# Kernel tuning notes

Measured on AMD Instinct MI355X. Metric: run time of the kernel, lower is better.

Reference implementation:

```python
import jax, jax.numpy as jnp
import numpy as np

PS = 32
D = 256


def setup_inputs() -> dict:
    key = jax.random.key(0)
    ks = jax.random.split(key, 9)
    B, L = 32, 32768
    s_in = 1.0 / np.sqrt(PS)
    s_d = 1.0 / np.sqrt(D)
    return {
        "x": jax.random.normal(ks[0], (B, L), dtype=jnp.float32),
        "W_proj": jax.random.normal(ks[1], (PS, D), dtype=jnp.float32) * s_in,
        "b_proj": jnp.zeros((D,), jnp.float32),
        "W_qkv": jax.random.normal(ks[2], (D, 3 * D), dtype=jnp.float32) * s_d,
        "b_qkv": jnp.zeros((3 * D,), jnp.float32),
        "W_out": jax.random.normal(ks[3], (D, D), dtype=jnp.float32) * s_d,
        "b_out": jnp.zeros((D,), jnp.float32),
        "W_head": jax.random.normal(ks[4], (D, PS), dtype=jnp.float32) * s_d,
        "b_head": jnp.zeros((PS,), jnp.float32),
    }


def reference(x, W_proj, b_proj, W_qkv, b_qkv, W_out, b_out, W_head, b_head):
    B, L = x.shape
    T = L // PS
    # InstanceNorm over full series (torch .std is unbiased -> ddof=1)
    mean = jnp.mean(x, axis=-1, keepdims=True)
    std = jnp.std(x, axis=-1, keepdims=True, ddof=1) + 1e-5
    x_norm = (x - mean) / std
    patches = x_norm.reshape(B, T, PS)
    # Patch embedding
    h = patches @ W_proj + b_proj  # [B, T, D]
    # Single-head causal self-attention (explicit scores, as in source)
    qkv = h @ W_qkv + b_qkv
    q, k, v = jnp.split(qkv, 3, axis=-1)
    scale = 1.0 / jnp.sqrt(jnp.asarray(D, dtype=h.dtype))
    attn = jnp.einsum("btd,bsd->bts", q, k) * scale  # [B, T, T]
    causal = jnp.tril(jnp.ones((T, T), dtype=bool))
    attn = jnp.where(causal, attn, -jnp.inf)
    attn = jax.nn.softmax(attn, axis=-1)
    out = jnp.einsum("bts,bsd->btd", attn, v)
    out = out @ W_out + b_out
    # Prediction head + next-patch MSE loss
    pred = out @ W_head + b_head  # [B, T, PS]
    loss = jnp.mean((pred[:, :-1] - patches[:, 1:]) ** 2)
    return loss
```

## Files before the change

kernel.cpp:

```cpp
#include <hip/hip_runtime.h>
#include <math.h>

#define B_SZ 32
#define L_SZ 32768
#define T_SZ 1024
#define PS_SZ 32
#define D_SZ 256
#define SM_M 10.0f

typedef float f32x4 __attribute__((ext_vector_type(4)));
typedef short s16x8 __attribute__((ext_vector_type(8)));
typedef unsigned short u16x8 __attribute__((ext_vector_type(8)));

__device__ __forceinline__ unsigned short f2bf(float f) {
  union { float f; unsigned int u; } v; v.f = f;
  unsigned int r = v.u + 0x7FFFu + ((v.u >> 16) & 1u);
  return (unsigned short)(r >> 16);
}

__device__ __forceinline__ void g2l16(const unsigned short* g, unsigned short* l) {
  __builtin_amdgcn_global_load_lds(
      (const __attribute__((address_space(1))) unsigned int*)g,
      (__attribute__((address_space(3))) unsigned int*)l, 16, 0, 0);
}

__global__ __launch_bounds__(256) void prep_kernel(const float* __restrict__ x,
                                                   float* __restrict__ sgpart,
                                                   const float* __restrict__ Wp,
                                                   const float* __restrict__ bp,
                                                   const float* __restrict__ Wq,
                                                   const float* __restrict__ bq,
                                                   const float* __restrict__ Wo,
                                                   const float* __restrict__ bo,
                                                   const float* __restrict__ Wh,
                                                   const float* __restrict__ bh,
                                                   float* __restrict__ Wcb,
                                                   unsigned short* __restrict__ WqT,
                                                   unsigned short* __restrict__ WfT,
                                                   float* __restrict__ bfp,
                                                   unsigned int* __restrict__ total,
                                                   float* __restrict__ lsum) {
  __shared__ float red[8];
  const int g = blockIdx.x, tid = threadIdx.x;
  const int w = tid >> 6, lane = tid & 63;
  if (g < 256) {
    const int b = g >> 3;
    const float* p = x + (size_t)b * L_SZ + (size_t)(g & 7) * 4096;
    float s = 0.f, ss = 0.f;
#pragma unroll
    for (int i = 0; i < 4; ++i) {
      float4 f = ((const float4*)p)[tid + i * 256];
      s += f.x + f.y + f.z + f.w;
      ss += f.x * f.x + f.y * f.y + f.z * f.z + f.w * f.w;
    }
#pragma unroll
    for (int off = 32; off >= 1; off >>= 1) {
      s += __shfl_down(s, off);
      ss += __shfl_down(ss, off);
    }
    if (lane == 0) { red[w] = s; red[4 + w] = ss; }
    __syncthreads();
    if (tid == 0) {
      sgpart[g * 2]     = red[0] + red[1] + red[2] + red[3];
      sgpart[g * 2 + 1] = red[4] + red[5] + red[6] + red[7];
    }
  } else if (g < 388) {
    int idx = (g - 256) * 256 + tid;
    if (idx < 33 * 768) {
      int p = idx / 768, j = idx % 768;
      const float* arow = (p < 32) ? (Wp + p * 256) : bp;
      float acc = (p < 32) ? 0.f : bq[j];
      for (int d = 0; d < 256; ++d) acc += arow[d] * Wq[d * 768 + j];
      if (p < 32) WqT[j * 32 + p] = f2bf(acc);
      else Wcb[j] = acc;
    } else {
      int k = idx - 33 * 768;
      if (k < 8192) {
        int p = k >> 8, d = k & 255;
        float acc = 0.f;
        for (int e = 0; e < 256; ++e) acc += Wo[d * 256 + e] * Wh[e * 32 + p];
        WfT[p * 256 + d] = f2bf(acc);
      } else if (k < 8224) {
        int p = k - 8192;
        float acc = bh[p];
        for (int e = 0; e < 256; ++e) acc += bo[e] * Wh[e * 32 + p];
        bfp[p] = acc;
      }
    }
  } else {
    if (tid == 0) { total[0] = 0u; lsum[0] = 0.f; }
  }
}

__global__ __launch_bounds__(256) void qkv_kernel(const float* __restrict__ x,
                                                  const float* __restrict__ sgpart,
                                                  const unsigned short* __restrict__ WqT,
                                                  const float* __restrict__ Wcb,
                                                  unsigned short* __restrict__ Qb,
                                                  unsigned short* __restrict__ Kb,
                                                  unsigned short* __restrict__ Vtt) {
  __shared__ unsigned short T4[4][8448];
  const int tid = threadIdx.x;
  const int w = tid >> 6, lane = tid & 63;
  const int lo = lane & 15, quad = lane >> 4;
  unsigned short* Tw = T4[w];
  const int mbase = blockIdx.x * 128 + w * 32;
  const int b = mbase >> 10;
  float S = 0.f, SS = 0.f;
#pragma unroll
  for (int i = 0; i < 8; ++i) {
    S += sgpart[(b * 8 + i) * 2];
    SS += sgpart[(b * 8 + i) * 2 + 1];
  }
  const float mean = S * (1.f / (float)L_SZ);
  const float var = (SS - S * mean) * (1.f / (float)(L_SZ - 1));
  const float inv = 1.f / (sqrtf(var) + 1e-5f);
  s16x8 af0, af1;
  {
    float4 a = *(const float4*)&x[(size_t)(mbase + lo) * 32 + quad * 8];
    float4 c = *(const float4*)&x[(size_t)(mbase + lo) * 32 + quad * 8 + 4];
    af0[0] = (short)f2bf((a.x - mean) * inv); af0[1] = (short)f2bf((a.y - mean) * inv);
    af0[2] = (short)f2bf((a.z - mean) * inv); af0[3] = (short)f2bf((a.w - mean) * inv);
    af0[4] = (short)f2bf((c.x - mean) * inv); af0[5] = (short)f2bf((c.y - mean) * inv);
    af0[6] = (short)f2bf((c.z - mean) * inv); af0[7] = (short)f2bf((c.w - mean) * inv);
    float4 d = *(const float4*)&x[(size_t)(mbase + 16 + lo) * 32 + quad * 8];
    float4 e = *(const float4*)&x[(size_t)(mbase + 16 + lo) * 32 + quad * 8 + 4];
    af1[0] = (short)f2bf((d.x - mean) * inv); af1[1] = (short)f2bf((d.y - mean) * inv);
    af1[2] = (short)f2bf((d.z - mean) * inv); af1[3] = (short)f2bf((d.w - mean) * inv);
    af1[4] = (short)f2bf((e.x - mean) * inv); af1[5] = (short)f2bf((e.y - mean) * inv);
    af1[6] = (short)f2bf((e.z - mean) * inv); af1[7] = (short)f2bf((e.w - mean) * inv);
  }
#pragma unroll 4
  for (int nt = 0; nt < 16; ++nt) {
    s16x8 bf = *(const s16x8*)&WqT[(size_t)(nt * 16 + lo) * 32 + quad * 8];
    f32x4 c0 = {0.f, 0.f, 0.f, 0.f}, c1 = {0.f, 0.f, 0.f, 0.f};
    c0 = __builtin_amdgcn_mfma_f32_16x16x32_bf16(af0, bf, c0, 0, 0, 0);
    c1 = __builtin_amdgcn_mfma_f32_16x16x32_bf16(af1, bf, c1, 0, 0, 0);
    const int col = nt * 16 + lo;
    const float bi = Wcb[col];
#pragma unroll
    for (int i = 0; i < 4; ++i) {
      Tw[(quad * 4 + i) * 264 + col]      = f2bf((c0[i] + bi) * 0.0625f);
      Tw[(16 + quad * 4 + i) * 264 + col] = f2bf((c1[i] + bi) * 0.0625f);
    }
  }
#pragma unroll
  for (int it = 0; it < 16; ++it) {
    const int gsub = it * 64 + lane;
    const int row = gsub >> 5, c16 = gsub & 31;
    *(u16x8*)&Qb[(size_t)(mbase + row) * 256 + c16 * 8] =
        *(const u16x8*)&Tw[row * 264 + c16 * 8];
  }
#pragma unroll 4
  for (int nt = 0; nt < 16; ++nt) {
    s16x8 bf = *(const s16x8*)&WqT[(size_t)(256 + nt * 16 + lo) * 32 + quad * 8];
    f32x4 c0 = {0.f, 0.f, 0.f, 0.f}, c1 = {0.f, 0.f, 0.f, 0.f};
    c0 = __builtin_amdgcn_mfma_f32_16x16x32_bf16(af0, bf, c0, 0, 0, 0);
    c1 = __builtin_amdgcn_mfma_f32_16x16x32_bf16(af1, bf, c1, 0, 0, 0);
    const int col = nt * 16 + lo;
    const float bi = Wcb[256 + col];
#pragma unroll
    for (int i = 0; i < 4; ++i) {
      Tw[(quad * 4 + i) * 264 + col]      = f2bf(c0[i] + bi);
      Tw[(16 + quad * 4 + i) * 264 + col] = f2bf(c1[i] + bi);
    }
  }
#pragma unroll
  for (int it = 0; it < 16; ++it) {
    const int gsub = it * 64 + lane;
    const int row = gsub >> 5, c16 = gsub & 31;
    *(u16x8*)&Kb[(size_t)(mbase + row) * 256 + c16 * 8] =
        *(const u16x8*)&Tw[row * 264 + c16 * 8];
  }
#pragma unroll 4
  for (int nt2 = 0; nt2 < 16; ++nt2) {
    s16x8 aw = *(const s16x8*)&WqT[(size_t)(512 + nt2 * 16 + lo) * 32 + quad * 8];
    f32x4 c0 = {0.f, 0.f, 0.f, 0.f}, c1 = {0.f, 0.f, 0.f, 0.f};
    c0 = __builtin_amdgcn_mfma_f32_16x16x32_bf16(aw, af0, c0, 0, 0, 0);
    c1 = __builtin_amdgcn_mfma_f32_16x16x32_bf16(aw, af1, c1, 0, 0, 0);
#pragma unroll
    for (int i = 0; i < 4; ++i) {
      const int d = nt2 * 16 + quad * 4 + i;
      const float bv = Wcb[512 + d];
      Tw[d * 32 + lo]      = f2bf(c0[i] + bv);
      Tw[d * 32 + 16 + lo] = f2bf(c1[i] + bv);
    }
  }
  {
    const int ktq = (mbase >> 5) & 31;
    const size_t vb = ((size_t)b * 32 + ktq) * 8192;
#pragma unroll
    for (int it = 0; it < 16; ++it) {
      const int gsub = it * 64 + lane;
      *(u16x8*)&Vtt[vb + gsub * 8] = *(const u16x8*)&Tw[gsub * 8];
    }
  }
}

__global__ __launch_bounds__(256) void attn_kernel(const unsigned short* __restrict__ Qb,
                                                   const unsigned short* __restrict__ Kb,
                                                   const unsigned short* __restrict__ Vtt,
                                                   const unsigned short* __restrict__ WfT,
                                                   const float* __restrict__ bfp,
                                                   const float* __restrict__ x,
                                                   const float* __restrict__ sgpart,
                                                   float* __restrict__ lsum,
                                                   unsigned int* __restrict__ total,
                                                   float* __restrict__ out) {
  __shared__ unsigned short SMEM[35328];
  const int g = blockIdx.x;
  const int j = g >> 3;
  const int b = (g & 7) * 4 + (j & 3);
  const int qt = 15 - (j >> 2);
  const int tid = threadIdx.x;
  const int w = tid >> 6, lane = tid & 63;
  const int lo = lane & 15, quad = lane >> 4;

  const int qr0 = qt * 64 + w * 16;
  const size_t kbase = (size_t)b << 10;

  s16x8 qf[8];
  const size_t qrow = (kbase + qr0 + lo) * 256;
#pragma unroll
  for (int kc = 0; kc < 8; ++kc) qf[kc] = *(const s16x8*)&Qb[qrow + kc * 32 + quad * 8];

  f32x4 O[16];
#pragma unroll
  for (int nt = 0; nt < 16; ++nt) O[nt] = (f32x4){0.f, 0.f, 0.f, 0.f};
  f32x4 Ol = {0.f, 0.f, 0.f, 0.f};
  s16x8 ones;
#pragma unroll
  for (int jj = 0; jj < 8; ++jj) ones[jj] = (short)0x3F80;

  const int c16p = tid & 31;
  const int keyr = tid >> 5;
  const int c16s = (c16p & 24) | ((c16p & 7) ^ keyr);
  const unsigned short* kgp = Kb + (kbase << 8) + keyr * 256 + c16s * 8;
  const int dql = tid >> 2;
  const int cpq = (tid & 3) ^ ((tid >> 3) & 3);
  const unsigned short* vgp = Vtt + (size_t)b * 262144 + dql * 32 + cpq * 8;
  const int ldst = (w * 64) * 8;

  unsigned short* myp = &SMEM[32768 + w * 640];
  const int lo7 = lo & 7;
  const int nk = 2 * (qt + 1);

#pragma unroll
  for (int it = 0; it < 4; ++it) g2l16(kgp + it * 2048, &SMEM[it * 2048 + ldst]);
#pragma unroll
  for (int it = 0; it < 4; ++it) g2l16(vgp + it * 2048, &SMEM[8192 + it * 2048 + ldst]);
  kgp += 8192; vgp += 8192;

  for (int kt = 0; kt < nk; ++kt) {
    const int k0 = kt * 32;
    __syncthreads();
    const int cur = (kt & 1) << 14;
    if (kt + 1 < nk) {
      const int nxt = ((kt + 1) & 1) << 14;
#pragma unroll
      for (int it = 0; it < 4; ++it) g2l16(kgp + it * 2048, &SMEM[nxt + it * 2048 + ldst]);
#pragma unroll
      for (int it = 0; it < 4; ++it)
        g2l16(vgp + it * 2048, &SMEM[nxt + 8192 + it * 2048 + ldst]);
      kgp += 8192; vgp += 8192;
    }

    if (k0 <= qr0 + 15) {
      f32x4 s0 = {0.f, 0.f, 0.f, 0.f}, s1 = {0.f, 0.f, 0.f, 0.f};
#pragma unroll
      for (int kc = 0; kc < 8; ++kc) {
        const int c16 = kc * 4 + quad;
        const int cs = (c16 & 24) | ((c16 & 7) ^ lo7);
        s16x8 kf0 = *(const s16x8*)&SMEM[cur + (lo * 32 + cs) * 8];
        s16x8 kf1 = *(const s16x8*)&SMEM[cur + ((16 + lo) * 32 + cs) * 8];
        s0 = __builtin_amdgcn_mfma_f32_16x16x32_bf16(qf[kc], kf0, s0, 0, 0, 0);
        s1 = __builtin_amdgcn_mfma_f32_16x16x32_bf16(qf[kc], kf1, s1, 0, 0, 0);
      }
      if (k0 + 31 > qr0) {
#pragma unroll
        for (int ii = 0; ii < 4; ++ii) {
          const int row = qr0 + quad * 4 + ii;
          if (k0 + lo > row) s0[ii] = -1e30f;
          if (k0 + 16 + lo > row) s1[ii] = -1e30f;
        }
      }
#pragma unroll
      for (int ii = 0; ii < 4; ++ii) {
        myp[(quad * 4 + ii) * 40 + lo]      = f2bf(__expf(s0[ii] - SM_M));
        myp[(quad * 4 + ii) * 40 + 16 + lo] = f2bf(__expf(s1[ii] - SM_M));
      }
      s16x8 pf = *(const s16x8*)&myp[lo * 40 + quad * 8];
      Ol = __builtin_amdgcn_mfma_f32_16x16x32_bf16(pf, ones, Ol, 0, 0, 0);
#pragma unroll
      for (int nt = 0; nt < 16; ++nt) {
        const int d = nt * 16 + lo;
        const int cp = quad ^ ((d >> 1) & 3);
        s16x8 vf = *(const s16x8*)&SMEM[cur + 8192 + ((d << 2) + cp) * 8];
        O[nt] = __builtin_amdgcn_mfma_f32_16x16x32_bf16(pf, vf, O[nt], 0, 0, 0);
      }
    }
  }
  __syncthreads();

  float inv4[4];
#pragma unroll
  for (int ii = 0; ii < 4; ++ii) inv4[ii] = 1.f / Ol[ii];
  unsigned short* OLw = &SMEM[w * 4224];
#pragma unroll
  for (int nt = 0; nt < 16; ++nt)
#pragma unroll
    for (int ii = 0; ii < 4; ++ii)
      OLw[(quad * 4 + ii) * 264 + nt * 16 + lo] = f2bf(O[nt][ii] * inv4[ii]);

  s16x8 af[8];
#pragma unroll
  for (int kc = 0; kc < 8; ++kc)
    af[kc] = *(const s16x8*)&OLw[lo * 264 + kc * 32 + quad * 8];

  float S = 0.f, SS = 0.f;
#pragma unroll
  for (int i = 0; i < 8; ++i) {
    S += sgpart[(b * 8 + i) * 2];
    SS += sgpart[(b * 8 + i) * 2 + 1];
  }
  const float mean = S * (1.f / (float)L_SZ);
  const float var = (SS - S * mean) * (1.f / (float)(L_SZ - 1));
  const float invb = 1.f / (sqrtf(var) + 1e-5f);

  float lacc = 0.f;
#pragma unroll
  for (int nt = 0; nt < 2; ++nt) {
    f32x4 acc = {0.f, 0.f, 0.f, 0.f};
#pragma unroll
    for (int kc = 0; kc < 8; ++kc) {
      s16x8 bfr = *(const s16x8*)&WfT[(size_t)(nt * 16 + lo) * 256 + kc * 32 + quad * 8];
      acc = __builtin_amdgcn_mfma_f32_16x16x32_bf16(af[kc], bfr, acc, 0, 0, 0);
    }
    const float ba = bfp[nt * 16 + lo];
    const int p = nt * 16 + lo;
#pragma unroll
    for (int ii = 0; ii < 4; ++ii) {
      const int t = qr0 + quad * 4 + ii;
      if (t < 1023) {
        const float pr = acc[ii] + ba;
        const float tg = (x[(size_t)b * L_SZ + (t + 1) * 32 + p] - mean) * invb;
        const float d = pr - tg;
        lacc += d * d;
      }
    }
  }
#pragma unroll
  for (int off = 32; off >= 1; off >>= 1) lacc += __shfl_down(lacc, off);
  float* redf = (float*)&SMEM[35000];
  unsigned int* flag = (unsigned int*)&SMEM[35100];
  if (lane == 0) redf[w] = lacc;
  __syncthreads();

  if (tid == 0) {
    atomicAdd(lsum, redf[0] + redf[1] + redf[2] + redf[3]);
    __threadfence();
    unsigned int prev = atomicAdd(total, 1u);
    flag[0] = (prev == 511u) ? 1u : 0u;
  }
  __syncthreads();
  if (flag[0] && tid == 0) {
    float tot = atomicAdd(lsum, 0.0f);
    out[0] = tot * (1.f / (float)(B_SZ * (T_SZ - 1) * PS_SZ));
  }
}

extern "C" void kernel_launch(void* const* d_in, const int* in_sizes, int n_in,
                              void* d_out, int out_size, void* d_ws, size_t ws_size,
                              hipStream_t stream) {
  const float* x      = (const float*)d_in[0];
  const float* W_proj = (const float*)d_in[1];
  const float* b_proj = (const float*)d_in[2];
  const float* W_qkv  = (const float*)d_in[3];
  const float* b_qkv  = (const float*)d_in[4];
  const float* W_out  = (const float*)d_in[5];
  const float* b_out  = (const float*)d_in[6];
  const float* W_head = (const float*)d_in[7];
  const float* b_head = (const float*)d_in[8];
  float* out = (float*)d_out;
  char* ws = (char*)d_ws;

  unsigned short* Qb     = (unsigned short*)ws;
  unsigned short* Kb     = (unsigned short*)(ws + (16ull << 20));
  unsigned short* Vtt    = (unsigned short*)(ws + (32ull << 20));
  char* tail = ws + (48ull << 20);
  float*          Wcb    = (float*)tail;
  unsigned short* WqT    = (unsigned short*)(tail + 4096);
  unsigned short* WfT    = (unsigned short*)(tail + 65536);
  float*          bfp    = (float*)(tail + 98304);
  float*          sgpart = (float*)(tail + 102400);
  unsigned int*   total  = (unsigned int*)(tail + 106496);
  float*          lsum   = (float*)(tail + 106496 + 64);

  prep_kernel<<<389, 256, 0, stream>>>(x, sgpart, W_proj, b_proj, W_qkv, b_qkv,
                                       W_out, b_out, W_head, b_head,
                                       Wcb, WqT, WfT, bfp, total, lsum);
  qkv_kernel<<<256, 256, 0, stream>>>(x, sgpart, WqT, Wcb, Qb, Kb, Vtt);
  attn_kernel<<<512, 256, 0, stream>>>(Qb, Kb, Vtt, WfT, bfp, x, sgpart, lsum, total, out);
}
```

Baseline: 163.2 us.

## Process two 16-row query tiles per wave in attention kernel

Each wave now computes 32 query rows using two MFMA M-tiles that share the same K and V fragments from LDS. Blocks cover 128 query rows and the grid is halved to 256 blocks, with the completion counter adjusted to match. This aims to halve K/V global and LDS traffic per query row. In exchange it raises accumulator register pressure, reduces the number of blocks and worsens causal load imbalance across CUs.

```diff
diff --git a/kernel.cpp b/kernel.cpp
--- a/kernel.cpp
+++ b/kernel.cpp
@@ -207,27 +207,32 @@
                                                    float* __restrict__ lsum,
                                                    unsigned int* __restrict__ total,
                                                    float* __restrict__ out) {
-  __shared__ unsigned short SMEM[35328];
+  __shared__ unsigned short SMEM[39040];
   const int g = blockIdx.x;
-  const int j = g >> 3;
-  const int b = (g & 7) * 4 + (j & 3);
-  const int qt = 15 - (j >> 2);
+  const int b = (g & 7) * 4 + ((g >> 3) & 3);
+  const int qt = 7 - (g >> 5);
   const int tid = threadIdx.x;
   const int w = tid >> 6, lane = tid & 63;
   const int lo = lane & 15, quad = lane >> 4;
 
-  const int qr0 = qt * 64 + w * 16;
+  const int qr0 = qt * 128 + w * 32;
   const size_t kbase = (size_t)b << 10;
 
-  s16x8 qf[8];
-  const size_t qrow = (kbase + qr0 + lo) * 256;
-#pragma unroll
-  for (int kc = 0; kc < 8; ++kc) qf[kc] = *(const s16x8*)&Qb[qrow + kc * 32 + quad * 8];
-
-  f32x4 O[16];
-#pragma unroll
-  for (int nt = 0; nt < 16; ++nt) O[nt] = (f32x4){0.f, 0.f, 0.f, 0.f};
-  f32x4 Ol = {0.f, 0.f, 0.f, 0.f};
+  s16x8 qf[2][8];
+#pragma unroll
+  for (int mt = 0; mt < 2; ++mt) {
+    const size_t qrow = (kbase + qr0 + mt * 16 + lo) * 256;
+#pragma unroll
+    for (int kc = 0; kc < 8; ++kc)
+      qf[mt][kc] = *(const s16x8*)&Qb[qrow + kc * 32 + quad * 8];
+  }
+
+  f32x4 O[2][16];
+#pragma unroll
+  for (int mt = 0; mt < 2; ++mt)
+#pragma unroll
+    for (int nt = 0; nt < 16; ++nt) O[mt][nt] = (f32x4){0.f, 0.f, 0.f, 0.f};
+  f32x4 Ol[2] = {{0.f, 0.f, 0.f, 0.f}, {0.f, 0.f, 0.f, 0.f}};
   s16x8 ones;
 #pragma unroll
   for (int jj = 0; jj < 8; ++jj) ones[jj] = (short)0x3F80;
@@ -241,9 +246,9 @@
   const unsigned short* vgp = Vtt + (size_t)b * 262144 + dql * 32 + cpq * 8;
   const int ldst = (w * 64) * 8;
 
-  unsigned short* myp = &SMEM[32768 + w * 640];
+  unsigned short* myp = &SMEM[32768 + w * 1280];
   const int lo7 = lo & 7;
-  const int nk = 2 * (qt + 1);
+  const int nk = 4 * qt + 4;
 
 #pragma unroll
   for (int it = 0; it < 4; ++it) g2l16(kgp + it * 2048, &SMEM[it * 2048 + ldst]);
@@ -265,57 +270,75 @@
       kgp += 8192; vgp += 8192;
     }
 
-    if (k0 <= qr0 + 15) {
-      f32x4 s0 = {0.f, 0.f, 0.f, 0.f}, s1 = {0.f, 0.f, 0.f, 0.f};
+    if (k0 <= qr0 + 31) {
+      f32x4 s[2][2];
+#pragma unroll
+      for (int mt = 0; mt < 2; ++mt)
+#pragma unroll
+        for (int nt = 0; nt < 2; ++nt) s[mt][nt] = (f32x4){0.f, 0.f, 0.f, 0.f};
 #pragma unroll
       for (int kc = 0; kc < 8; ++kc) {
         const int c16 = kc * 4 + quad;
         const int cs = (c16 & 24) | ((c16 & 7) ^ lo7);
         s16x8 kf0 = *(const s16x8*)&SMEM[cur + (lo * 32 + cs) * 8];
         s16x8 kf1 = *(const s16x8*)&SMEM[cur + ((16 + lo) * 32 + cs) * 8];
-        s0 = __builtin_amdgcn_mfma_f32_16x16x32_bf16(qf[kc], kf0, s0, 0, 0, 0);
-        s1 = __builtin_amdgcn_mfma_f32_16x16x32_bf16(qf[kc], kf1, s1, 0, 0, 0);
+        s[0][0] = __builtin_amdgcn_mfma_f32_16x16x32_bf16(qf[0][kc], kf0, s[0][0], 0, 0, 0);
+        s[0][1] = __builtin_amdgcn_mfma_f32_16x16x32_bf16(qf[0][kc], kf1, s[0][1], 0, 0, 0);
+        s[1][0] = __builtin_amdgcn_mfma_f32_16x16x32_bf16(qf[1][kc], kf0, s[1][0], 0, 0, 0);
+        s[1][1] = __builtin_amdgcn_mfma_f32_16x16x32_bf16(qf[1][kc], kf1, s[1][1], 0, 0, 0);
       }
       if (k0 + 31 > qr0) {
 #pragma unroll
+        for (int mt = 0; mt < 2; ++mt)
+#pragma unroll
+          for (int ii = 0; ii < 4; ++ii) {
+            const int row = qr0 + mt * 16 + quad * 4 + ii;
+            if (k0 + lo > row) s[mt][0][ii] = -1e30f;
+            if (k0 + 16 + lo > row) s[mt][1][ii] = -1e30f;
+          }
+      }
+#pragma unroll
+      for (int mt = 0; mt < 2; ++mt)
+#pragma unroll
         for (int ii = 0; ii < 4; ++ii) {
-          const int row = qr0 + quad * 4 + ii;
-          if (k0 + lo > row) s0[ii] = -1e30f;
-          if (k0 + 16 + lo > row) s1[ii] = -1e30f;
+          myp[(mt * 16 + quad * 4 + ii) * 40 + lo]      = f2bf(__expf(s[mt][0][ii] - SM_M));
+          myp[(mt * 16 + quad * 4 + ii) * 40 + 16 + lo] = f2bf(__expf(s[mt][1][ii] - SM_M));
         }
-      }
-#pragma unroll
-      for (int ii = 0; ii < 4; ++ii) {
-        myp[(quad * 4 + ii) * 40 + lo]      = f2bf(__expf(s0[ii] - SM_M));
-        myp[(quad * 4 + ii) * 40 + 16 + lo] = f2bf(__expf(s1[ii] - SM_M));
-      }
-      s16x8 pf = *(const s16x8*)&myp[lo * 40 + quad * 8];
-      Ol = __builtin_amdgcn_mfma_f32_16x16x32_bf16(pf, ones, Ol, 0, 0, 0);
+      s16x8 pf0 = *(const s16x8*)&myp[lo * 40 + quad * 8];
+      s16x8 pf1 = *(const s16x8*)&myp[(16 + lo) * 40 + quad * 8];
+      Ol[0] = __builtin_amdgcn_mfma_f32_16x16x32_bf16(pf0, ones, Ol[0], 0, 0, 0);
+      Ol[1] = __builtin_amdgcn_mfma_f32_16x16x32_bf16(pf1, ones, Ol[1], 0, 0, 0);
 #pragma unroll
       for (int nt = 0; nt < 16; ++nt) {
         const int d = nt * 16 + lo;
         const int cp = quad ^ ((d >> 1) & 3);
         s16x8 vf = *(const s16x8*)&SMEM[cur + 8192 + ((d << 2) + cp) * 8];
-        O[nt] = __builtin_amdgcn_mfma_f32_16x16x32_bf16(pf, vf, O[nt], 0, 0, 0);
+        O[0][nt] = __builtin_amdgcn_mfma_f32_16x16x32_bf16(pf0, vf, O[0][nt], 0, 0, 0);
+        O[1][nt] = __builtin_amdgcn_mfma_f32_16x16x32_bf16(pf1, vf, O[1][nt], 0, 0, 0);
       }
     }
   }
   __syncthreads();
 
-  float inv4[4];
-#pragma unroll
-  for (int ii = 0; ii < 4; ++ii) inv4[ii] = 1.f / Ol[ii];
-  unsigned short* OLw = &SMEM[w * 4224];
-#pragma unroll
-  for (int nt = 0; nt < 16; ++nt)
-#pragma unroll
-    for (int ii = 0; ii < 4; ++ii)
-      OLw[(quad * 4 + ii) * 264 + nt * 16 + lo] = f2bf(O[nt][ii] * inv4[ii]);
-
-  s16x8 af[8];
-#pragma unroll
-  for (int kc = 0; kc < 8; ++kc)
-    af[kc] = *(const s16x8*)&OLw[lo * 264 + kc * 32 + quad * 8];
+  unsigned short* OLw = &SMEM[w * 8448];
+#pragma unroll
+  for (int mt = 0; mt < 2; ++mt) {
+    float inv4[4];
+#pragma unroll
+    for (int ii = 0; ii < 4; ++ii) inv4[ii] = 1.f / Ol[mt][ii];
+#pragma unroll
+    for (int nt = 0; nt < 16; ++nt)
+#pragma unroll
+      for (int ii = 0; ii < 4; ++ii)
+        OLw[(mt * 16 + quad * 4 + ii) * 264 + nt * 16 + lo] = f2bf(O[mt][nt][ii] * inv4[ii]);
+  }
+
+  s16x8 af[2][8];
+#pragma unroll
+  for (int kc = 0; kc < 8; ++kc) {
+    af[0][kc] = *(const s16x8*)&OLw[lo * 264 + kc * 32 + quad * 8];
+    af[1][kc] = *(const s16x8*)&OLw[(16 + lo) * 264 + kc * 32 + quad * 8];
+  }
 
   float S = 0.f, SS = 0.f;
 #pragma unroll
@@ -330,29 +353,37 @@
   float lacc = 0.f;
 #pragma unroll
   for (int nt = 0; nt < 2; ++nt) {
-    f32x4 acc = {0.f, 0.f, 0.f, 0.f};
+    f32x4 acc0 = {0.f, 0.f, 0.f, 0.f}, acc1 = {0.f, 0.f, 0.f, 0.f};
 #pragma unroll
     for (int kc = 0; kc < 8; ++kc) {
       s16x8 bfr = *(const s16x8*)&WfT[(size_t)(nt * 16 + lo) * 256 + kc * 32 + quad * 8];
-      acc = __builtin_amdgcn_mfma_f32_16x16x32_bf16(af[kc], bfr, acc, 0, 0, 0);
+      acc0 = __builtin_amdgcn_mfma_f32_16x16x32_bf16(af[0][kc], bfr, acc0, 0, 0, 0);
+      acc1 = __builtin_amdgcn_mfma_f32_16x16x32_bf16(af[1][kc], bfr, acc1, 0, 0, 0);
     }
     const float ba = bfp[nt * 16 + lo];
     const int p = nt * 16 + lo;
 #pragma unroll
     for (int ii = 0; ii < 4; ++ii) {
-      const int t = qr0 + quad * 4 + ii;
-      if (t < 1023) {
-        const float pr = acc[ii] + ba;
-        const float tg = (x[(size_t)b * L_SZ + (t + 1) * 32 + p] - mean) * invb;
+      const int t0 = qr0 + quad * 4 + ii;
+      if (t0 < 1023) {
+        const float pr = acc0[ii] + ba;
+        const float tg = (x[(size_t)b * L_SZ + (t0 + 1) * 32 + p] - mean) * invb;
         const float d = pr - tg;
         lacc += d * d;
       }
+      const int t1 = qr0 + 16 + quad * 4 + ii;
+      if (t1 < 1023) {
+        const float pr = acc1[ii] + ba;
+        const float tg = (x[(size_t)b * L_SZ + (t1 + 1) * 32 + p] - mean) * invb;
+        const float d = pr - tg;
+        lacc += d * d;
+      }
     }
   }
 #pragma unroll
   for (int off = 32; off >= 1; off >>= 1) lacc += __shfl_down(lacc, off);
-  float* redf = (float*)&SMEM[35000];
-  unsigned int* flag = (unsigned int*)&SMEM[35100];
+  float* redf = (float*)&SMEM[38912];
+  unsigned int* flag = (unsigned int*)&SMEM[38960];
   if (lane == 0) redf[w] = lacc;
   __syncthreads();
 
@@ -360,7 +391,7 @@
     atomicAdd(lsum, redf[0] + redf[1] + redf[2] + redf[3]);
     __threadfence();
     unsigned int prev = atomicAdd(total, 1u);
-    flag[0] = (prev == 511u) ? 1u : 0u;
+    flag[0] = (prev == 255u) ? 1u : 0u;
   }
   __syncthreads();
   if (flag[0] && tid == 0) {
@@ -400,5 +431,5 @@
                                        W_out, b_out, W_head, b_head,
                                        Wcb, WqT, WfT, bfp, total, lsum);
   qkv_kernel<<<256, 256, 0, stream>>>(x, sgpart, WqT, Wcb, Qb, Kb, Vtt);
-  attn_kernel<<<512, 256, 0, stream>>>(Qb, Kb, Vtt, WfT, bfp, x, sgpart, lsum, total, out);
-}
+  attn_kernel<<<256, 256, 0, stream>>>(Qb, Kb, Vtt, WfT, bfp, x, sgpart, lsum, total, out);
+}
```

Result: slower. 184.5 us (+13.1%).

## Halve attention block size to 32 query rows and drop K/V double buffering

Applied to the files above, without the earlier changes.

The attention kernel now runs 1024 blocks of 128 threads, each covering 32 query rows instead of 64, with half the LDS footprint. The double-buffered K/V prefetch is replaced by single-buffered loads bracketed by two barriers, and the per-wave causal skip check is removed since every wave now needs every loaded tile. The aim is more resident blocks per CU and finer load balance across the causal triangle. The cost is that load latency is no longer overlapped with compute, each K/V tile is loaded by twice as many blocks, and there are extra syncs per tile.

```diff
diff --git a/kernel.cpp b/kernel.cpp
--- a/kernel.cpp
+++ b/kernel.cpp
@@ -197,7 +197,7 @@
   }
 }
 
-__global__ __launch_bounds__(256) void attn_kernel(const unsigned short* __restrict__ Qb,
+__global__ __launch_bounds__(128) void attn_kernel(const unsigned short* __restrict__ Qb,
                                                    const unsigned short* __restrict__ Kb,
                                                    const unsigned short* __restrict__ Vtt,
                                                    const unsigned short* __restrict__ WfT,
@@ -207,16 +207,15 @@
                                                    float* __restrict__ lsum,
                                                    unsigned int* __restrict__ total,
                                                    float* __restrict__ out) {
-  __shared__ unsigned short SMEM[35328];
+  __shared__ unsigned short SMEM[17728];
   const int g = blockIdx.x;
-  const int j = g >> 3;
-  const int b = (g & 7) * 4 + (j & 3);
-  const int qt = 15 - (j >> 2);
+  const int b = (g & 7) * 4 + ((g >> 3) & 3);
+  const int qt = 31 - (g >> 5);
   const int tid = threadIdx.x;
   const int w = tid >> 6, lane = tid & 63;
   const int lo = lane & 15, quad = lane >> 4;
 
-  const int qr0 = qt * 64 + w * 16;
+  const int qr0 = qt * 32 + w * 16;
   const size_t kbase = (size_t)b << 10;
 
   s16x8 qf[8];
@@ -232,47 +231,40 @@
 #pragma unroll
   for (int jj = 0; jj < 8; ++jj) ones[jj] = (short)0x3F80;
 
+  const int k5 = tid >> 5;
   const int c16p = tid & 31;
-  const int keyr = tid >> 5;
-  const int c16s = (c16p & 24) | ((c16p & 7) ^ keyr);
-  const unsigned short* kgp = Kb + (kbase << 8) + keyr * 256 + c16s * 8;
-  const int dql = tid >> 2;
+  const int c16sA = (c16p & 24) | ((c16p & 7) ^ k5);
+  const int c16sB = c16sA ^ 4;
+  const unsigned short* kgpA = Kb + (kbase << 8) + k5 * 256 + c16sA * 8;
+  const unsigned short* kgpB = Kb + (kbase << 8) + (4 + k5) * 256 + c16sB * 8;
   const int cpq = (tid & 3) ^ ((tid >> 3) & 3);
-  const unsigned short* vgp = Vtt + (size_t)b * 262144 + dql * 32 + cpq * 8;
-  const int ldst = (w * 64) * 8;
-
-  unsigned short* myp = &SMEM[32768 + w * 640];
+  const unsigned short* vgp = Vtt + (size_t)b * 262144 + (tid >> 2) * 32 + cpq * 8;
+
+  unsigned short* myp = &SMEM[16384 + w * 640];
   const int lo7 = lo & 7;
-  const int nk = 2 * (qt + 1);
-
-#pragma unroll
-  for (int it = 0; it < 4; ++it) g2l16(kgp + it * 2048, &SMEM[it * 2048 + ldst]);
-#pragma unroll
-  for (int it = 0; it < 4; ++it) g2l16(vgp + it * 2048, &SMEM[8192 + it * 2048 + ldst]);
-  kgp += 8192; vgp += 8192;
+  const int nk = qt + 1;
 
   for (int kt = 0; kt < nk; ++kt) {
     const int k0 = kt * 32;
     __syncthreads();
-    const int cur = (kt & 1) << 14;
-    if (kt + 1 < nk) {
-      const int nxt = ((kt + 1) & 1) << 14;
-#pragma unroll
-      for (int it = 0; it < 4; ++it) g2l16(kgp + it * 2048, &SMEM[nxt + it * 2048 + ldst]);
-#pragma unroll
-      for (int it = 0; it < 4; ++it)
-        g2l16(vgp + it * 2048, &SMEM[nxt + 8192 + it * 2048 + ldst]);
-      kgp += 8192; vgp += 8192;
-    }
-
-    if (k0 <= qr0 + 15) {
+#pragma unroll
+    for (int it2 = 0; it2 < 4; ++it2) {
+      g2l16(kgpA + (size_t)kt * 8192 + it2 * 2048, &SMEM[(it2 * 256 + w * 64) * 8]);
+      g2l16(kgpB + (size_t)kt * 8192 + it2 * 2048, &SMEM[((it2 * 256 + 128) + w * 64) * 8]);
+    }
+#pragma unroll
+    for (int it = 0; it < 8; ++it)
+      g2l16(vgp + (size_t)kt * 8192 + it * 1024, &SMEM[8192 + (it * 128 + w * 64) * 8]);
+    __syncthreads();
+
+    {
       f32x4 s0 = {0.f, 0.f, 0.f, 0.f}, s1 = {0.f, 0.f, 0.f, 0.f};
 #pragma unroll
       for (int kc = 0; kc < 8; ++kc) {
         const int c16 = kc * 4 + quad;
         const int cs = (c16 & 24) | ((c16 & 7) ^ lo7);
-        s16x8 kf0 = *(const s16x8*)&SMEM[cur + (lo * 32 + cs) * 8];
-        s16x8 kf1 = *(const s16x8*)&SMEM[cur + ((16 + lo) * 32 + cs) * 8];
+        s16x8 kf0 = *(const s16x8*)&SMEM[(lo * 32 + cs) * 8];
+        s16x8 kf1 = *(const s16x8*)&SMEM[((16 + lo) * 32 + cs) * 8];
         s0 = __builtin_amdgcn_mfma_f32_16x16x32_bf16(qf[kc], kf0, s0, 0, 0, 0);
         s1 = __builtin_amdgcn_mfma_f32_16x16x32_bf16(qf[kc], kf1, s1, 0, 0, 0);
       }
@@ -295,7 +287,7 @@
       for (int nt = 0; nt < 16; ++nt) {
         const int d = nt * 16 + lo;
         const int cp = quad ^ ((d >> 1) & 3);
-        s16x8 vf = *(const s16x8*)&SMEM[cur + 8192 + ((d << 2) + cp) * 8];
+        s16x8 vf = *(const s16x8*)&SMEM[8192 + ((d << 2) + cp) * 8];
         O[nt] = __builtin_amdgcn_mfma_f32_16x16x32_bf16(pf, vf, O[nt], 0, 0, 0);
       }
     }
@@ -351,16 +343,16 @@
   }
 #pragma unroll
   for (int off = 32; off >= 1; off >>= 1) lacc += __shfl_down(lacc, off);
-  float* redf = (float*)&SMEM[35000];
-  unsigned int* flag = (unsigned int*)&SMEM[35100];
+  float* redf = (float*)&SMEM[17664];
+  unsigned int* flag = (unsigned int*)&SMEM[17696];
   if (lane == 0) redf[w] = lacc;
   __syncthreads();
 
   if (tid == 0) {
-    atomicAdd(lsum, redf[0] + redf[1] + redf[2] + redf[3]);
+    atomicAdd(lsum, redf[0] + redf[1]);
     __threadfence();
     unsigned int prev = atomicAdd(total, 1u);
-    flag[0] = (prev == 511u) ? 1u : 0u;
+    flag[0] = (prev == 1023u) ? 1u : 0u;
   }
   __syncthreads();
   if (flag[0] && tid == 0) {
@@ -400,5 +392,5 @@
                                        W_out, b_out, W_head, b_head,
                                        Wcb, WqT, WfT, bfp, total, lsum);
   qkv_kernel<<<256, 256, 0, stream>>>(x, sgpart, WqT, Wcb, Qb, Kb, Vtt);
-  attn_kernel<<<512, 256, 0, stream>>>(Qb, Kb, Vtt, WfT, bfp, x, sgpart, lsum, total, out);
-}
+  attn_kernel<<<1024, 128, 0, stream>>>(Qb, Kb, Vtt, WfT, bfp, x, sgpart, lsum, total, out);
+}
```

Result: slower. 176.3 us (+8.0%).
